# Kernel tuning notes

Hardware: AMD Instinct MI355X
Metric: run time of the kernel (lower is better)

## Reference

```python
import jax, jax.numpy as jnp
import numpy as np

NEG_INF = -1.0e9  # matches torch code's masked fill value


def setup_inputs() -> dict:
    key = jax.random.key(0)
    k1, k2, k3, k4 = jax.random.split(key, 4)
    n, q, s, d, v = 8, 4096, 4096, 64, 64
    return {
        "queries_nqd": jax.random.normal(k1, (n, q, d), dtype=jnp.float32),
        "keys_nsd": jax.random.normal(k2, (n, s, d), dtype=jnp.float32),
        "values_nsv": jax.random.normal(k3, (n, s, v), dtype=jnp.float32),
        "attention_mask_nqs": jax.random.randint(k4, (n, q, s), 0, 2).astype(jnp.bool_),
    }


def reference(queries_nqd, keys_nsd, values_nsv, attention_mask_nqs):
    d = queries_nqd.shape[-1]
    scale = 1.0 / jnp.sqrt(jnp.asarray(d, dtype=queries_nqd.dtype))
    # [n,q,s] = [n,q,d] @ [n,d,s]
    scores_nqs = jnp.einsum("nqd,nsd->nqs", queries_nqd, keys_nsd) * scale
    scores_nqs = jnp.where(attention_mask_nqs, scores_nqs, jnp.asarray(NEG_INF, scores_nqs.dtype))
    probs_nqs = jax.nn.softmax(scores_nqs, axis=-1)
    # dropout p=0.0 (eval) -> identity
    return jnp.einsum("nqs,nsv->nqv", probs_nqs, values_nsv)
```

## Files before the change

### kernel.cpp

```cpp
#include <hip/hip_runtime.h>
#include <hip/hip_bf16.h>


#define NHEADS 8
#define QLEN   4096
#define SLEN   4096
#define DDIM   64
#define VDIM   64
#define SBLK   64
#define QBLK   128
#define NWAVES 8
#define NCHUNK (SLEN / SBLK)

typedef __bf16          bf16x4 __attribute__((ext_vector_type(4)));
typedef __bf16          bf16x8 __attribute__((ext_vector_type(8)));
typedef float           f32x4  __attribute__((ext_vector_type(4)));
typedef unsigned int    u32x4  __attribute__((ext_vector_type(4)));
typedef unsigned short  u16x4  __attribute__((ext_vector_type(4)));

#define KSWZ(s) (((s) & 7) << 4)
#define VSWZ(v) ((((v) >> 2) & 7) << 4)
#define CLAMPC(c) ((c) < NCHUNK ? (c) : NCHUNK - 1)

#define LDS_BARRIER() do {                                          \
  asm volatile("s_waitcnt lgkmcnt(0)" ::: "memory");                \
  __builtin_amdgcn_s_barrier();                                     \
  __builtin_amdgcn_sched_barrier(0);                                \
} while (0)

__device__ __forceinline__ int detect_mfmt(const unsigned char* __restrict__ M) {
  const int lane = threadIdx.x & 63;
  u32x4 w = *((const u32x4*)M + lane);
  unsigned o = w[0] | w[1] | w[2] | w[3];
  unsigned comb = ((o & 0x00FFFF00u) ? 1u : 0u) | ((o & 0x000000FFu) ? 2u : 0u);
  comb |= __shfl_xor((int)comb, 1);  comb |= __shfl_xor((int)comb, 2);
  comb |= __shfl_xor((int)comb, 4);  comb |= __shfl_xor((int)comb, 8);
  comb |= __shfl_xor((int)comb, 16); comb |= __shfl_xor((int)comb, 32);
  return ((comb & 1u) == 0u) ? 1 : (((comb & 2u) == 0u) ? 2 : 0);
}

template<bool U8>
__global__ __launch_bounds__(512, 2)
void attn_fwd(const float* __restrict__ Qg, const float* __restrict__ Kg,
              const float* __restrict__ Vg, const unsigned char* __restrict__ Mg,
              float* __restrict__ Og)
{
  __shared__ __align__(16) unsigned short Ksh[2][64 * 64];
  __shared__ __align__(16) unsigned short Vsh[2][64 * 64];
  __shared__ __align__(16) unsigned short Psh[NWAVES][16 * 64];

  {
    const int mfmt = detect_mfmt(Mg);
    if (U8 ? (mfmt != 0) : (mfmt == 0)) return;
  }

  const int tid  = threadIdx.x;
  const int wave = tid >> 6;
  const int lane = tid & 63;
  const int g    = lane >> 4;
  const int lq   = lane & 15;

  const int head = blockIdx.x;
  const int qblk = blockIdx.y;

  const float* Qp = Qg + ((size_t)head * QLEN + (size_t)qblk * QBLK) * DDIM;
  const float* Kp = Kg + (size_t)head * SLEN * DDIM;
  const float* Vp = Vg + (size_t)head * SLEN * VDIM;
  float* Op = Og + ((size_t)head * QLEN + (size_t)qblk * QBLK) * DDIM;

  const float QSCALE = 0.125f * 1.44269504f;
  const int qrow = wave * 16 + lq;
  bf16x8 qf[2];
#pragma unroll
  for (int ks = 0; ks < 2; ++ks) {
    const float* qp = Qp + (size_t)qrow * DDIM + 8 * g + 32 * ks;
    f32x4 a = *(const f32x4*)qp;
    f32x4 b = *(const f32x4*)(qp + 4);
    bf16x8 t;
#pragma unroll
    for (int j = 0; j < 4; ++j) { t[j] = (__bf16)(a[j] * QSCALE); t[4 + j] = (__bf16)(b[j] * QSCALE); }
    qf[ks] = t;
  }

  const size_t mrow_elems = ((size_t)head * QLEN + (size_t)qblk * QBLK + qrow) * SLEN;
  const unsigned char* mrow8  = Mg + mrow_elems;
  const unsigned*      mrow32 = (const unsigned*)Mg + mrow_elems;

  f32x4 oacc[4];
#pragma unroll
  for (int vt = 0; vt < 4; ++vt) oacc[vt] = (f32x4){0.f, 0.f, 0.f, 0.f};
  float m_run = -INFINITY;
  float l_run = 0.f;

  f32x4 kpA[2], vpA[2], kpB[2], vpB[2];
  unsigned m8A[4],  m8B[4];
  u32x4    m32A[4], m32B[4];

#define PREFETCH_KV(C, KP, VP)                                                 \
  _Pragma("unroll")                                                            \
  for (int it = 0; it < 2; ++it) {                                             \
    int srow = (tid >> 4) + it * 32;                                           \
    int d0   = (tid & 15) * 4;                                                 \
    size_t gs = (size_t)(CLAMPC(C) * SBLK + srow);                             \
    KP[it] = *(const f32x4*)(Kp + gs * DDIM + d0);                             \
    VP[it] = *(const f32x4*)(Vp + gs * VDIM + d0);                             \
  }

#define WRITE_KV(BUF, KP, VP)                                                  \
  _Pragma("unroll")                                                            \
  for (int it = 0; it < 2; ++it) {                                             \
    int srow = (tid >> 4) + it * 32;                                           \
    int d0   = (tid & 15) * 4;                                                 \
    bf16x4 kb;                                                                 \
    _Pragma("unroll") for (int j = 0; j < 4; ++j) kb[j] = (__bf16)KP[it][j];   \
    int koff = (srow * 128 + d0 * 2) ^ KSWZ(srow);                             \
    *(u16x4*)((char*)Ksh[BUF] + koff) = __builtin_bit_cast(u16x4, kb);         \
    _Pragma("unroll")                                                          \
    for (int j = 0; j < 4; ++j) {                                              \
      int v = d0 + j;                                                          \
      unsigned short b = __builtin_bit_cast(unsigned short, (__bf16)VP[it][j]); \
      int voff = (v * 128 + srow * 2) ^ VSWZ(v);                               \
      *(unsigned short*)((char*)Vsh[BUF] + voff) = b;                          \
    }                                                                          \
  }

#define LOAD_MASK(M8, M32, C)                                                  \
  if constexpr (U8) {                                                          \
    _Pragma("unroll")                                                          \
    for (int st = 0; st < 4; ++st)                                             \
      M8[st] = *(const unsigned*)(mrow8 + (size_t)CLAMPC(C) * SBLK + 16 * st + 4 * g); \
  } else {                                                                     \
    _Pragma("unroll")                                                          \
    for (int st = 0; st < 4; ++st)                                             \
      M32[st] = *(const u32x4*)(mrow32 + (size_t)CLAMPC(C) * SBLK + 16 * st + 4 * g); \
  }

#define CHUNK_BODY(C, CUR, KPF, VPF, KPW, VPW, M8U, M32U) {                    \
  PREFETCH_KV((C) + 2, KPF, VPF);                                              \
                               \
  f32x4 sacc[4];                                                               \
  _Pragma("unroll")                                                            \
  for (int st = 0; st < 4; ++st) sacc[st] = (f32x4){0.f, 0.f, 0.f, 0.f};       \
  __builtin_amdgcn_s_setprio(1);                                               \
  _Pragma("unroll")                                                            \
  for (int st = 0; st < 4; ++st) {                                             \
    int srow = lq + 16 * st;                                                   \
    _Pragma("unroll")                                                          \
    for (int ks = 0; ks < 2; ++ks) {                                           \
      int off = (srow * 128 + (8 * g + 32 * ks) * 2) ^ KSWZ(srow);             \
      bf16x8 kf = *(const bf16x8*)((const char*)Ksh[CUR] + off);               \
      sacc[st] = __builtin_amdgcn_mfma_f32_16x16x32_bf16(kf, qf[ks], sacc[st], 0, 0, 0); \
    }                                                                          \
  }                                                                            \
  __builtin_amdgcn_s_setprio(0);                                               \
                      \
  float vals[4][4];                                                            \
  float mloc = -INFINITY;                                                      \
  _Pragma("unroll")                                                            \
  for (int st = 0; st < 4; ++st) {                                             \
    bool keep[4];                                                              \
    if constexpr (U8) {                                                        \
      _Pragma("unroll")                                                        \
      for (int r = 0; r < 4; ++r) keep[r] = ((M8U[st] >> (8 * r)) & 0xFFu) != 0u; \
    } else {                                                                   \
      _Pragma("unroll")                                                        \
      for (int r = 0; r < 4; ++r) keep[r] = M32U[st][r] != 0u;                 \
    }                                                                          \
    _Pragma("unroll")                                                          \
    for (int r = 0; r < 4; ++r) {                                              \
      float v = keep[r] ? sacc[st][r] : -1.0e9f;                               \
      vals[st][r] = v;                                                         \
      mloc = fmaxf(mloc, v);                                                   \
    }                                                                          \
  }                                                                            \
  LOAD_MASK(M8U, M32U, (C) + 2);            \
  mloc = fmaxf(mloc, __shfl_xor(mloc, 16));                                    \
  mloc = fmaxf(mloc, __shfl_xor(mloc, 32));                                    \
      \
  if (!__all(mloc <= m_run + 8.0f)) {                                          \
    float m_new = fmaxf(m_run, mloc);                                          \
    float alpha = __builtin_amdgcn_exp2f(m_run - m_new);                       \
    l_run *= alpha;                                                            \
    _Pragma("unroll")                                                          \
    for (int vt = 0; vt < 4; ++vt) {                                           \
      _Pragma("unroll")                                                        \
      for (int r = 0; r < 4; ++r) oacc[vt][r] *= alpha;                        \
    }                                                                          \
    m_run = m_new;                                                             \
  }                                                                            \
  float lsum = 0.f;                                                            \
  _Pragma("unroll")                                                            \
  for (int st = 0; st < 4; ++st) {                                             \
    bf16x4 pb;                                                                 \
    _Pragma("unroll")                                                          \
    for (int r = 0; r < 4; ++r) {                                              \
      float p = __builtin_amdgcn_exp2f(vals[st][r] - m_run);                   \
      lsum += p;                                                               \
      pb[r] = (__bf16)p;                                                       \
    }                                                                          \
    int off = (lq * 128 + (16 * st + 4 * g) * 2) ^ KSWZ(lq);                   \
    *(u16x4*)((char*)Psh[wave] + off) = __builtin_bit_cast(u16x4, pb);         \
  }                                                                            \
  lsum += __shfl_xor(lsum, 16);                                                \
  lsum += __shfl_xor(lsum, 32);                                                \
  l_run += lsum;                                                               \
                                                \
  __builtin_amdgcn_s_setprio(1);                                               \
  _Pragma("unroll")                                                            \
  for (int ks = 0; ks < 2; ++ks) {                                             \
    int poff = (lq * 128 + (8 * g + 32 * ks) * 2) ^ KSWZ(lq);                  \
    bf16x8 pf = *(const bf16x8*)((const char*)Psh[wave] + poff);               \
    _Pragma("unroll")                                                          \
    for (int vt = 0; vt < 4; ++vt) {                                           \
      int vrow = lq + 16 * vt;                                                 \
      int voff = (vrow * 128 + (8 * g + 32 * ks) * 2) ^ VSWZ(vrow);            \
      bf16x8 vf = *(const bf16x8*)((const char*)Vsh[CUR] + voff);              \
      oacc[vt] = __builtin_amdgcn_mfma_f32_16x16x32_bf16(vf, pf, oacc[vt], 0, 0, 0); \
    }                                                                          \
  }                                                                            \
  __builtin_amdgcn_s_setprio(0);                                               \
  WRITE_KV((CUR) ^ 1, KPW, VPW);         \
  LDS_BARRIER();                                                               \
}

  PREFETCH_KV(0, kpA, vpA);
  LOAD_MASK(m8A, m32A, 0);
  PREFETCH_KV(1, kpB, vpB);
  LOAD_MASK(m8B, m32B, 1);
  WRITE_KV(0, kpA, vpA);
  LDS_BARRIER();

  for (int cc = 0; cc < NCHUNK; cc += 2) {
    CHUNK_BODY(cc,     0, kpA, vpA, kpB, vpB, m8A, m32A);
    CHUNK_BODY(cc + 1, 1, kpB, vpB, kpA, vpA, m8B, m32B);
  }

  float inv_l = 1.0f / l_run;
  float* orow = Op + (size_t)qrow * VDIM;
#pragma unroll
  for (int vt = 0; vt < 4; ++vt) {
    f32x4 o;
#pragma unroll
    for (int r = 0; r < 4; ++r) o[r] = oacc[vt][r] * inv_l;
    *(f32x4*)(orow + 16 * vt + 4 * g) = o;
  }
#undef PREFETCH_KV
#undef WRITE_KV
#undef LOAD_MASK
#undef CHUNK_BODY
}

extern "C" void kernel_launch(void* const* d_in, const int* in_sizes, int n_in,
                              void* d_out, int out_size, void* d_ws, size_t ws_size,
                              hipStream_t stream) {
  const float* Qg = (const float*)d_in[0];
  const float* Kg = (const float*)d_in[1];
  const float* Vg = (const float*)d_in[2];
  const unsigned char* Mg = (const unsigned char*)d_in[3];
  float* Og = (float*)d_out;

  dim3 grid(NHEADS, QLEN / QBLK);
  dim3 block(512);
  attn_fwd<true ><<<grid, block, 0, stream>>>(Qg, Kg, Vg, Mg, Og);
  attn_fwd<false><<<grid, block, 0, stream>>>(Qg, Kg, Vg, Mg, Og);
}
```

Measured before the change: 148.0 us.

## Switch to 32x32x16 MFMA with split-S waves and LDS merge of partial softmax

Each block's waves are reorganized so that 4 query tiles of 32 rows are each covered by two waves, and each wave handles one half of every 64-key chunk. The 16x16x32 MFMAs are replaced with 32x32x16 MFMAs for both QK^T and PV, which reduces LDS fragment loads per FLOP and drops one cross-lane shuffle from the max and sum reductions. At the end, the two partial (m, l, O) states for each query tile are merged through new LDS buffers. This adds LDS footprint and an extra barrier, and the larger accumulators raise register pressure.

```diff
diff --git a/kernel.cpp b/kernel.cpp
--- a/kernel.cpp
+++ b/kernel.cpp
@@ -9,17 +9,18 @@
 #define VDIM   64
 #define SBLK   64
 #define QBLK   128
-#define NWAVES 8
 #define NCHUNK (SLEN / SBLK)
 
 typedef __bf16          bf16x4 __attribute__((ext_vector_type(4)));
 typedef __bf16          bf16x8 __attribute__((ext_vector_type(8)));
 typedef float           f32x4  __attribute__((ext_vector_type(4)));
+typedef float           f32x16 __attribute__((ext_vector_type(16)));
 typedef unsigned int    u32x4  __attribute__((ext_vector_type(4)));
 typedef unsigned short  u16x4  __attribute__((ext_vector_type(4)));
 
 #define KSWZ(s) (((s) & 7) << 4)
 #define VSWZ(v) ((((v) >> 2) & 7) << 4)
+#define PSWZ(q) (((q) & 3) << 4)
 #define CLAMPC(c) ((c) < NCHUNK ? (c) : NCHUNK - 1)
 
 #define LDS_BARRIER() do {                                          \
@@ -27,6 +28,13 @@
   __builtin_amdgcn_s_barrier();                                     \
   __builtin_amdgcn_sched_barrier(0);                                \
 } while (0)
+
+__device__ __forceinline__ f32x16 zero16() {
+  f32x16 z;
+#pragma unroll
+  for (int i = 0; i < 16; ++i) z[i] = 0.f;
+  return z;
+}
 
 __device__ __forceinline__ int detect_mfmt(const unsigned char* __restrict__ M) {
   const int lane = threadIdx.x & 63;
@@ -47,18 +55,22 @@
 {
   __shared__ __align__(16) unsigned short Ksh[2][64 * 64];
   __shared__ __align__(16) unsigned short Vsh[2][64 * 64];
-  __shared__ __align__(16) unsigned short Psh[NWAVES][16 * 64];
+  __shared__ __align__(16) unsigned short Psh[8][32 * 32];
+  __shared__ __align__(16) float mO[4][32][68];
+  __shared__            float mM[4][2][32];
 
   {
     const int mfmt = detect_mfmt(Mg);
     if (U8 ? (mfmt != 0) : (mfmt == 0)) return;
   }
 
-  const int tid  = threadIdx.x;
-  const int wave = tid >> 6;
-  const int lane = tid & 63;
-  const int g    = lane >> 4;
-  const int lq   = lane & 15;
+  const int tid   = threadIdx.x;
+  const int wave  = tid >> 6;
+  const int lane  = tid & 63;
+  const int qtile = wave & 3;
+  const int shalf = wave >> 2;
+  const int lq    = lane & 31;
+  const int h     = lane >> 5;
 
   const int head = blockIdx.x;
   const int qblk = blockIdx.y;
@@ -69,26 +81,26 @@
   float* Op = Og + ((size_t)head * QLEN + (size_t)qblk * QBLK) * DDIM;
 
   const float QSCALE = 0.125f * 1.44269504f;
-  const int qrow = wave * 16 + lq;
-  bf16x8 qf[2];
-#pragma unroll
-  for (int ks = 0; ks < 2; ++ks) {
-    const float* qp = Qp + (size_t)qrow * DDIM + 8 * g + 32 * ks;
+  const int qrow = qtile * 32 + lq;
+  bf16x8 qf[4];
+#pragma unroll
+  for (int kd = 0; kd < 4; ++kd) {
+    const float* qp = Qp + (size_t)qrow * DDIM + 16 * kd + 8 * h;
     f32x4 a = *(const f32x4*)qp;
     f32x4 b = *(const f32x4*)(qp + 4);
     bf16x8 t;
 #pragma unroll
     for (int j = 0; j < 4; ++j) { t[j] = (__bf16)(a[j] * QSCALE); t[4 + j] = (__bf16)(b[j] * QSCALE); }
-    qf[ks] = t;
-  }
-
-  const size_t mrow_elems = ((size_t)head * QLEN + (size_t)qblk * QBLK + qrow) * SLEN;
-  const unsigned char* mrow8  = Mg + mrow_elems;
-  const unsigned*      mrow32 = (const unsigned*)Mg + mrow_elems;
-
-  f32x4 oacc[4];
-#pragma unroll
-  for (int vt = 0; vt < 4; ++vt) oacc[vt] = (f32x4){0.f, 0.f, 0.f, 0.f};
+    qf[kd] = t;
+  }
+
+  const size_t mbase = ((size_t)head * QLEN + (size_t)qblk * QBLK + qrow) * SLEN
+                     + (size_t)shalf * 32;
+  const unsigned char* mrow8  = Mg + mbase;
+  const unsigned*      mrow32 = (const unsigned*)Mg + mbase;
+
+  f32x16 oacc[2];
+  oacc[0] = zero16(); oacc[1] = zero16();
   float m_run = -INFINITY;
   float l_run = 0.f;
 
@@ -128,32 +140,27 @@
   if constexpr (U8) {                                                          \
     _Pragma("unroll")                                                          \
     for (int st = 0; st < 4; ++st)                                             \
-      M8[st] = *(const unsigned*)(mrow8 + (size_t)CLAMPC(C) * SBLK + 16 * st + 4 * g); \
+      M8[st] = *(const unsigned*)(mrow8 + (size_t)CLAMPC(C) * SBLK + 8 * st + 4 * h); \
   } else {                                                                     \
     _Pragma("unroll")                                                          \
     for (int st = 0; st < 4; ++st)                                             \
-      M32[st] = *(const u32x4*)(mrow32 + (size_t)CLAMPC(C) * SBLK + 16 * st + 4 * g); \
+      M32[st] = *(const u32x4*)(mrow32 + (size_t)CLAMPC(C) * SBLK + 8 * st + 4 * h); \
   }
 
 #define CHUNK_BODY(C, CUR, KPF, VPF, KPW, VPW, M8U, M32U) {                    \
   PREFETCH_KV((C) + 2, KPF, VPF);                                              \
-                               \
-  f32x4 sacc[4];                                                               \
-  _Pragma("unroll")                                                            \
-  for (int st = 0; st < 4; ++st) sacc[st] = (f32x4){0.f, 0.f, 0.f, 0.f};       \
+       \
+  f32x16 sacc = zero16();                                                      \
   __builtin_amdgcn_s_setprio(1);                                               \
   _Pragma("unroll")                                                            \
-  for (int st = 0; st < 4; ++st) {                                             \
-    int srow = lq + 16 * st;                                                   \
-    _Pragma("unroll")                                                          \
-    for (int ks = 0; ks < 2; ++ks) {                                           \
-      int off = (srow * 128 + (8 * g + 32 * ks) * 2) ^ KSWZ(srow);             \
-      bf16x8 kf = *(const bf16x8*)((const char*)Ksh[CUR] + off);               \
-      sacc[st] = __builtin_amdgcn_mfma_f32_16x16x32_bf16(kf, qf[ks], sacc[st], 0, 0, 0); \
-    }                                                                          \
+  for (int kd = 0; kd < 4; ++kd) {                                             \
+    int srow = shalf * 32 + lq;                                                \
+    int off = (srow * 128 + (32 * kd + 16 * h)) ^ KSWZ(srow);                  \
+    bf16x8 kf = *(const bf16x8*)((const char*)Ksh[CUR] + off);                 \
+    sacc = __builtin_amdgcn_mfma_f32_32x32x16_bf16(kf, qf[kd], sacc, 0, 0, 0); \
   }                                                                            \
   __builtin_amdgcn_s_setprio(0);                                               \
-                      \
+               \
   float vals[4][4];                                                            \
   float mloc = -INFINITY;                                                      \
   _Pragma("unroll")                                                            \
@@ -168,13 +175,12 @@
     }                                                                          \
     _Pragma("unroll")                                                          \
     for (int r = 0; r < 4; ++r) {                                              \
-      float v = keep[r] ? sacc[st][r] : -1.0e9f;                               \
+      float v = keep[r] ? sacc[4 * st + r] : -1.0e9f;                          \
       vals[st][r] = v;                                                         \
       mloc = fmaxf(mloc, v);                                                   \
     }                                                                          \
   }                                                                            \
   LOAD_MASK(M8U, M32U, (C) + 2);            \
-  mloc = fmaxf(mloc, __shfl_xor(mloc, 16));                                    \
   mloc = fmaxf(mloc, __shfl_xor(mloc, 32));                                    \
       \
   if (!__all(mloc <= m_run + 8.0f)) {                                          \
@@ -182,9 +188,9 @@
     float alpha = __builtin_amdgcn_exp2f(m_run - m_new);                       \
     l_run *= alpha;                                                            \
     _Pragma("unroll")                                                          \
-    for (int vt = 0; vt < 4; ++vt) {                                           \
+    for (int vt = 0; vt < 2; ++vt) {                                           \
       _Pragma("unroll")                                                        \
-      for (int r = 0; r < 4; ++r) oacc[vt][r] *= alpha;                        \
+      for (int r = 0; r < 16; ++r) oacc[vt][r] *= alpha;                       \
     }                                                                          \
     m_run = m_new;                                                             \
   }                                                                            \
@@ -198,24 +204,24 @@
       lsum += p;                                                               \
       pb[r] = (__bf16)p;                                                       \
     }                                                                          \
-    int off = (lq * 128 + (16 * st + 4 * g) * 2) ^ KSWZ(lq);                   \
-    *(u16x4*)((char*)Psh[wave] + off) = __builtin_bit_cast(u16x4, pb);         \
-  }                                                                            \
-  lsum += __shfl_xor(lsum, 16);                                                \
+    int poff = (lq * 64 + (16 * st + 8 * h)) ^ PSWZ(lq);                       \
+    *(unsigned long long*)((char*)Psh[wave] + poff) =                          \
+        __builtin_bit_cast(unsigned long long, pb);                            \
+  }                                                                            \
   lsum += __shfl_xor(lsum, 32);                                                \
   l_run += lsum;                                                               \
-                                                \
+               \
   __builtin_amdgcn_s_setprio(1);                                               \
   _Pragma("unroll")                                                            \
-  for (int ks = 0; ks < 2; ++ks) {                                             \
-    int poff = (lq * 128 + (8 * g + 32 * ks) * 2) ^ KSWZ(lq);                  \
+  for (int ks2 = 0; ks2 < 2; ++ks2) {                                          \
+    int poff = (lq * 64 + (32 * ks2 + 16 * h)) ^ PSWZ(lq);                     \
     bf16x8 pf = *(const bf16x8*)((const char*)Psh[wave] + poff);               \
     _Pragma("unroll")                                                          \
-    for (int vt = 0; vt < 4; ++vt) {                                           \
-      int vrow = lq + 16 * vt;                                                 \
-      int voff = (vrow * 128 + (8 * g + 32 * ks) * 2) ^ VSWZ(vrow);            \
+    for (int vt = 0; vt < 2; ++vt) {                                           \
+      int vrow = vt * 32 + lq;                                                 \
+      int voff = (vrow * 128 + (64 * shalf + 32 * ks2 + 16 * h)) ^ VSWZ(vrow); \
       bf16x8 vf = *(const bf16x8*)((const char*)Vsh[CUR] + voff);              \
-      oacc[vt] = __builtin_amdgcn_mfma_f32_16x16x32_bf16(vf, pf, oacc[vt], 0, 0, 0); \
+      oacc[vt] = __builtin_amdgcn_mfma_f32_32x32x16_bf16(vf, pf, oacc[vt], 0, 0, 0); \
     }                                                                          \
   }                                                                            \
   __builtin_amdgcn_s_setprio(0);                                               \
@@ -235,14 +241,44 @@
     CHUNK_BODY(cc + 1, 1, kpB, vpB, kpA, vpA, m8B, m32B);
   }
 
-  float inv_l = 1.0f / l_run;
-  float* orow = Op + (size_t)qrow * VDIM;
-#pragma unroll
-  for (int vt = 0; vt < 4; ++vt) {
-    f32x4 o;
-#pragma unroll
-    for (int r = 0; r < 4; ++r) o[r] = oacc[vt][r] * inv_l;
-    *(f32x4*)(orow + 16 * vt + 4 * g) = o;
+  if (shalf == 1) {
+#pragma unroll
+    for (int vt = 0; vt < 2; ++vt) {
+#pragma unroll
+      for (int st = 0; st < 4; ++st) {
+        int v0 = 32 * vt + 8 * st + 4 * h;
+        f32x4 o;
+#pragma unroll
+        for (int r = 0; r < 4; ++r) o[r] = oacc[vt][4 * st + r];
+        *(f32x4*)&mO[qtile][lq][v0] = o;
+      }
+    }
+    if (h == 0) {
+      mM[qtile][0][lq] = m_run;
+      mM[qtile][1][lq] = l_run;
+    }
+  }
+  LDS_BARRIER();
+  if (shalf == 0) {
+    float m1 = mM[qtile][0][lq];
+    float l1 = mM[qtile][1][lq];
+    float mm = fmaxf(m_run, m1);
+    float a0 = __builtin_amdgcn_exp2f(m_run - mm);
+    float a1 = __builtin_amdgcn_exp2f(m1 - mm);
+    float inv = 1.0f / (l_run * a0 + l1 * a1);
+    float* orow = Op + (size_t)qrow * VDIM;
+#pragma unroll
+    for (int vt = 0; vt < 2; ++vt) {
+#pragma unroll
+      for (int st = 0; st < 4; ++st) {
+        int v0 = 32 * vt + 8 * st + 4 * h;
+        f32x4 o1 = *(const f32x4*)&mO[qtile][lq][v0];
+        f32x4 o;
+#pragma unroll
+        for (int r = 0; r < 4; ++r) o[r] = (oacc[vt][4 * st + r] * a0 + o1[r] * a1) * inv;
+        *(f32x4*)(orow + v0) = o;
+      }
+    }
   }
 #undef PREFETCH_KV
 #undef WRITE_KV
```

New measurement: 150.2 us. About the same (+1.4%).
